# Performance work log

Measured on AMD Instinct MI355X. Metric: run time of the kernel, lower is better.

## Reference

```python
import jax, jax.numpy as jnp
import numpy as np

B, C, H, W = 16, 192, 48, 48
EPS = 1e-5  # torch LayerNorm default


def setup_inputs() -> dict:
    key = jax.random.key(0)
    ks = jax.random.split(key, 5)
    dim = C
    x = jax.random.normal(ks[0], (B, C, H, W), dtype=jnp.float32)
    ln_w = jnp.ones((dim,), dtype=jnp.float32)
    ln_b = jnp.zeros((dim,), dtype=jnp.float32)
    s = 1.0 / np.sqrt(dim)
    Wq = jax.random.uniform(ks[1], (dim, dim), jnp.float32, -s, s)
    Wk = jax.random.uniform(ks[2], (dim, dim), jnp.float32, -s, s)
    Wv = jax.random.uniform(ks[3], (dim, dim), jnp.float32, -s, s)
    w1 = jnp.ones((1,), dtype=jnp.float32)
    w2 = jnp.ones((1,), dtype=jnp.float32)
    return {"x": x, "ln_w": ln_w, "ln_b": ln_b, "Wq": Wq, "Wk": Wk, "Wv": Wv, "w1": w1, "w2": w2}


def reference(x, ln_w, ln_b, Wq, Wk, Wv, w1, w2):
    b, c, h, w = x.shape
    # [B, C, H, W] -> [B, N, C]
    xf = x.reshape(b, c, h * w).transpose(0, 2, 1)
    # LayerNorm over channel dim
    mu = jnp.mean(xf, axis=-1, keepdims=True)
    var = jnp.mean(jnp.square(xf - mu), axis=-1, keepdims=True)
    xn = (xf - mu) * jax.lax.rsqrt(var + EPS) * ln_w + ln_b
    # torch Linear: y = x @ W^T
    Q = jnp.einsum('bnc,dc->bnd', xn, Wq)
    K = jnp.einsum('bnc,dc->bnd', xn, Wk)
    V = jnp.einsum('bnc,dc->bnd', xn, Wv)
    S = jnp.einsum('bnd,bmd->bnm', Q, K)  # [B, N, N]
    attn1 = jax.nn.softmax(S, axis=-1)
    attn2 = jnp.square(jax.nn.relu(S))
    # learned blend weights (softmax over two scalars)
    e1, e2 = jnp.exp(w1), jnp.exp(w2)
    denom = e1 + e2
    attn = (e1 / denom) * attn1 + (e2 / denom) * attn2
    out = jnp.einsum('bnm,bmd->bnd', attn, V)  # [B, N, C]
    out = out.transpose(0, 2, 1).reshape(b, c, h, w)
    return out + x
```

## Files before the change

### kernel.cpp

```cpp
#include <hip/hip_runtime.h>

#define NN 2304
#define CC 192
#define NBATCH 16

typedef unsigned short u16;
typedef __bf16 bf16x8 __attribute__((ext_vector_type(8)));
typedef float f32x4 __attribute__((ext_vector_type(4)));
typedef float f32x16 __attribute__((ext_vector_type(16)));

__device__ __forceinline__ u16 bf16bits(float f) {
  union { float f; unsigned u; } v;
  v.f = f;
  unsigned r = v.u + 0x7FFFu + ((v.u >> 16) & 1u);
  return (u16)(r >> 16);
}

__device__ __forceinline__ uint32_t cvtpk(float lo, float hi) {
  uint32_t d;
  asm("v_cvt_pk_bf16_f32 %0, %1, %2" : "=v"(d) : "v"(lo), "v"(hi));
  return d;
}

__device__ __forceinline__ int swzK(int row, int col) {
  int ch = col >> 3;
  int phys = (ch & ~7) | ((ch ^ row) & 7);
  return row * 192 + (phys << 3) + (col & 7);
}
__device__ __forceinline__ int swz64(int row, int col) {
  int ch = (col >> 3) ^ row;
  return (row << 6) | ((ch & 7) << 3) | (col & 7);
}

__device__ __forceinline__ void gll16(const u16* g, u16* l) {
  __builtin_amdgcn_global_load_lds(
      (const __attribute__((address_space(1))) u16*)g,
      (__attribute__((address_space(3))) u16*)l, 16, 0, 0);
}

__global__ __launch_bounds__(256) void ln_kernel(
    const float* __restrict__ x, const float* __restrict__ lnw,
    const float* __restrict__ lnb, u16* __restrict__ xn) {
  __shared__ float xt[192 * 65];
  __shared__ float psum[4][64], psq[4][64];
  __shared__ float mu_s[64], rs_s[64];
  __shared__ float lw_s[192], lb_s[192];
  int t = threadIdx.x;
  int b = blockIdx.y, n0 = blockIdx.x * 64;
  const float* xb = x + (size_t)b * CC * NN;
  if (t < 192) { lw_s[t] = lnw[t]; lb_s[t] = lnb[t]; }
#pragma unroll
  for (int i = 0; i < 48; ++i) {
    int idx = i * 256 + t;
    int c = idx >> 6, n = idx & 63;
    xt[c * 65 + n] = xb[(size_t)c * NN + n0 + n];
  }
  __syncthreads();
  {
    int n = t & 63, part = t >> 6;
    float s = 0.f, s2 = 0.f;
#pragma unroll
    for (int c = part * 48; c < part * 48 + 48; ++c) {
      float v = xt[c * 65 + n];
      s += v; s2 += v * v;
    }
    psum[part][n] = s; psq[part][n] = s2;
  }
  __syncthreads();
  if (t < 64) {
    float s = psum[0][t] + psum[1][t] + psum[2][t] + psum[3][t];
    float s2 = psq[0][t] + psq[1][t] + psq[2][t] + psq[3][t];
    float mu = s * (1.0f / 192.0f);
    float var = s2 * (1.0f / 192.0f) - mu * mu;
    mu_s[t] = mu;
    rs_s[t] = rsqrtf(var + 1e-5f);
  }
  __syncthreads();
#pragma unroll
  for (int i = 0; i < 12; ++i) {
    int u = i * 256 + t;
    int n = u / 48, cq = (u % 48) * 4;
    float mu = mu_s[n], rs = rs_s[n];
    float v0 = (xt[(cq + 0) * 65 + n] - mu) * rs * lw_s[cq + 0] + lb_s[cq + 0];
    float v1 = (xt[(cq + 1) * 65 + n] - mu) * rs * lw_s[cq + 1] + lb_s[cq + 1];
    float v2 = (xt[(cq + 2) * 65 + n] - mu) * rs * lw_s[cq + 2] + lb_s[cq + 2];
    float v3 = (xt[(cq + 3) * 65 + n] - mu) * rs * lw_s[cq + 3] + lb_s[cq + 3];
    uint2 o;
    o.x = cvtpk(v0, v1);
    o.y = cvtpk(v2, v3);
    *(uint2*)&xn[((size_t)(b * NN + n0 + n)) * CC + cq] = o;
  }
}

__global__ __launch_bounds__(256, 3) void qkv_gemm(
    const u16* __restrict__ xn, const float* __restrict__ Wq,
    const float* __restrict__ Wk, const float* __restrict__ Wv,
    u16* __restrict__ qb, u16* __restrict__ kb, u16* __restrict__ vtb) {
  __shared__ u16 xs[12288];
  __shared__ u16 wsm[12288];
  int t = threadIdx.x, w = t >> 6, lane = t & 63, l15 = lane & 15, qd = lane >> 4;
  int m0 = blockIdx.x * 64, n0 = blockIdx.y * 64, z = blockIdx.z;
  const float* W = (z == 0) ? Wq : (z == 1 ? Wk : Wv);
#pragma unroll
  for (int i = 0; i < 6; ++i) {
    int ch = i * 256 + t;
    int row = ch / 24, cin = (ch % 24) * 8;
    *(uint4*)&xs[swzK(row, cin)] = *(const uint4*)&xn[(size_t)(m0 + row) * 192 + cin];
  }
#pragma unroll
  for (int i = 0; i < 6; ++i) {
    int ch = i * 256 + t;
    int row = ch / 24, cin = (ch % 24) * 8;
    const float* src = &W[(size_t)(n0 + row) * 192 + cin];
    float4 f0 = *(const float4*)src;
    float4 f1 = *(const float4*)(src + 4);
    uint4 o;
    o.x = cvtpk(f0.x, f0.y);
    o.y = cvtpk(f0.z, f0.w);
    o.z = cvtpk(f1.x, f1.y);
    o.w = cvtpk(f1.z, f1.w);
    *(uint4*)&wsm[swzK(row, cin)] = o;
  }
  __syncthreads();
  bf16x8 a[6];
#pragma unroll
  for (int kk = 0; kk < 6; ++kk)
    a[kk] = *(const bf16x8*)&xs[swzK(w * 16 + l15, kk * 32 + qd * 8)];
  const f32x4 fz = {0.f, 0.f, 0.f, 0.f};
  f32x4 acc[4];
#pragma unroll
  for (int ct = 0; ct < 4; ++ct) {
    acc[ct] = fz;
#pragma unroll
    for (int kk = 0; kk < 6; ++kk) {
      bf16x8 bfr = *(const bf16x8*)&wsm[swzK(ct * 16 + l15, kk * 32 + qd * 8)];
      acc[ct] = __builtin_amdgcn_mfma_f32_16x16x32_bf16(a[kk], bfr, acc[ct], 0, 0, 0);
    }
  }
  if (z < 2) {
    u16* outp = (z == 0) ? qb : kb;
#pragma unroll
    for (int ct = 0; ct < 4; ++ct)
#pragma unroll
      for (int r = 0; r < 4; ++r) {
        int m = m0 + w * 16 + qd * 4 + r;
        outp[(size_t)m * 192 + n0 + ct * 16 + l15] = bf16bits(acc[ct][r]);
      }
  } else {
    __syncthreads();
#pragma unroll
    for (int ct = 0; ct < 4; ++ct)
#pragma unroll
      for (int r = 0; r < 4; ++r)
        xs[swz64(ct * 16 + l15, w * 16 + qd * 4 + r)] = bf16bits(acc[ct][r]);
    __syncthreads();
    int b = blockIdx.x / 36, nb = (blockIdx.x % 36) * 64;
#pragma unroll
    for (int i = 0; i < 16; ++i) {
      int idx = i * 256 + t;
      int d = idx >> 6, nn = idx & 63;
      vtb[(size_t)b * 192 * NN + (size_t)(n0 + d) * NN + nb + nn] = xs[swz64(d, nn)];
    }
  }
}

__global__ __launch_bounds__(256, 2) void attn_fused(
    const u16* __restrict__ qb, const u16* __restrict__ kb,
    const u16* __restrict__ vtb, const float* __restrict__ w1p,
    const float* __restrict__ w2p, const float* __restrict__ x,
    float* __restrict__ out) {
  __shared__ u16 sm[32768];
  float* olds = (float*)sm;
  float* lred = (float*)(sm + 24576);

  int t = threadIdx.x, w = t >> 6, lane = t & 63;
  int l31 = lane & 31, hi = lane >> 5;
  int qh = w >> 1, ch = w & 1;
  int bid = blockIdx.x;
  int xcd = bid & 7, j = bid >> 3;
  int b = xcd * 2 + (j >= 36 ? 1 : 0);
  int qt = (j >= 36) ? j - 36 : j;

  const u16* Kg = kb + (size_t)b * NN * CC;
  const u16* Vg = vtb + (size_t)b * CC * NN;
  const u16* Qr = qb + ((size_t)b * NN + qt * 64 + qh * 32 + l31) * CC + hi * 8;
  bf16x8 qf[12];
#pragma unroll
  for (int ks = 0; ks < 12; ++ks) qf[ks] = *(const bf16x8*)(Qr + ks * 16);

  float e1 = __expf(w1p[0]), e2 = __expf(w2p[0]);
  float den = e1 + e2;
  float c1f = e1 / den, c2f = e2 / den;

  u16* pexSW = sm + 24576 + (qh * 2 + ch) * 1024 + lane * 8;
  const u16* pexSR = sm + 24576 + (qh * 2 + (1 - ch)) * 1024 + lane * 8;
  u16* pexRW = sm + 28672 + (qh * 2 + ch) * 1024 + lane * 8;
  const u16* pexRR = sm + 28672 + (qh * 2 + (1 - ch)) * 1024 + lane * 8;

  f32x16 z16;
#pragma unroll
  for (int i = 0; i < 16; ++i) z16[i] = 0.f;
  f32x16 os[3], orl[3];
#pragma unroll
  for (int i = 0; i < 3; ++i) { os[i] = z16; orl[i] = z16; }
  float lsum = 0.f;

#define STAGE_K(KT)                                                        \
  {                                                                        \
    _Pragma("unroll") for (int i = 0; i < 6; ++i) {                        \
      int cid = i * 4 + w, sc = cid * 64 + lane;                           \
      int row = sc / 24, pc = sc % 24;                                     \
      int gc = (pc & ~7) | ((pc ^ row) & 7);                               \
      gll16(Kg + ((size_t)(KT) * 64 + row) * CC + gc * 8, sm + cid * 512); \
    }                                                                      \
  }
#define STAGE_V(KT)                                                        \
  {                                                                        \
    _Pragma("unroll") for (int i = 0; i < 6; ++i) {                        \
      int cid = i * 4 + w, sc = cid * 64 + lane;                           \
      int d = sc >> 3, pc = sc & 7, gc = (pc ^ d) & 7;                     \
      gll16(Vg + (size_t)d * NN + (KT) * 64 + gc * 8,                      \
            sm + 12288 + cid * 512);                                       \
    }                                                                      \
  }

  alignas(16) uint32_t pS0[4], pS1[4], pR0[4], pR1[4];
#define S_BLEND()                                                           \
  {                                                                         \
    f32x16 sA0 = z16, sA1 = z16;                                            \
    __builtin_amdgcn_s_setprio(1);                                          \
    _Pragma("unroll") for (int ks = 0; ks < 6; ++ks) {                      \
      bf16x8 k0 =                                                           \
          *(const bf16x8*)&sm[swzK(ch * 32 + l31, (2 * ks) * 16 + hi * 8)]; \
      bf16x8 k1 =                                                           \
          *(const bf16x8*)&sm[swzK(ch * 32 + l31, (2 * ks + 1) * 16 + hi * 8)]; \
      sA0 = __builtin_amdgcn_mfma_f32_32x32x16_bf16(k0, qf[2 * ks], sA0, 0, 0, 0); \
      sA1 = __builtin_amdgcn_mfma_f32_32x32x16_bf16(k1, qf[2 * ks + 1], sA1, 0, 0, 0); \
    }                                                                       \
    __builtin_amdgcn_s_setprio(0);                                          \
    uint32_t WS[8], WR[8];                                                  \
    _Pragma("unroll") for (int g = 0; g < 4; ++g) {                         \
      float sv0 = sA0[4 * g + 0] + sA1[4 * g + 0];                          \
      float sv1 = sA0[4 * g + 1] + sA1[4 * g + 1];                          \
      float sv2 = sA0[4 * g + 2] + sA1[4 * g + 2];                          \
      float sv3 = sA0[4 * g + 3] + sA1[4 * g + 3];                          \
      float e0 = __expf(fminf(sv0, 60.f));                                  \
      float e1v = __expf(fminf(sv1, 60.f));                                 \
      float e2v = __expf(fminf(sv2, 60.f));                                 \
      float e3 = __expf(fminf(sv3, 60.f));                                  \
      float r0 = fmaxf(sv0, 0.f), r1 = fmaxf(sv1, 0.f);                     \
      float r2 = fmaxf(sv2, 0.f), r3 = fmaxf(sv3, 0.f);                     \
      lsum += (e0 + e1v) + (e2v + e3);                                      \
      WS[2 * g] = cvtpk(e0, e1v);                                           \
      WS[2 * g + 1] = cvtpk(e2v, e3);                                       \
      WR[2 * g] = cvtpk(r0 * r0, r1 * r1);                                  \
      WR[2 * g + 1] = cvtpk(r2 * r2, r3 * r3);                              \
    }                                                                       \
    uint32_t XS[8], XR[8];                                                  \
    _Pragma("unroll") for (int jj = 0; jj < 8; ++jj) {                      \
      XS[jj] = __shfl_xor(WS[jj], 32);                                      \
      XR[jj] = __shfl_xor(WR[jj], 32);                                      \
    }                                                                       \
    pS0[0] = hi ? XS[2] : WS[0]; pS0[1] = hi ? XS[3] : WS[1];               \
    pS0[2] = hi ? WS[2] : XS[0]; pS0[3] = hi ? WS[3] : XS[1];               \
    pS1[0] = hi ? XS[6] : WS[4]; pS1[1] = hi ? XS[7] : WS[5];               \
    pS1[2] = hi ? WS[6] : XS[4]; pS1[3] = hi ? WS[7] : XS[5];               \
    pR0[0] = hi ? XR[2] : WR[0]; pR0[1] = hi ? XR[3] : WR[1];               \
    pR0[2] = hi ? WR[2] : XR[0]; pR0[3] = hi ? WR[3] : XR[1];               \
    pR1[0] = hi ? XR[6] : WR[4]; pR1[1] = hi ? XR[7] : WR[5];               \
    pR1[2] = hi ? WR[6] : XR[4]; pR1[3] = hi ? WR[7] : XR[5];               \
    *(uint4*)pexSW = *(uint4*)pS0;                                          \
    *(uint4*)(pexSW + 512) = *(uint4*)pS1;                                  \
    *(uint4*)pexRW = *(uint4*)pR0;                                          \
    *(uint4*)(pexRW + 512) = *(uint4*)pR1;                                  \
  }

  STAGE_K(0);
  STAGE_V(0);
  asm volatile("s_waitcnt vmcnt(6)\ns_barrier" ::: "memory");
  S_BLEND();
  asm volatile("s_waitcnt lgkmcnt(0)\ns_barrier" ::: "memory");
  STAGE_K(1);

  for (int kt = 0; kt < 36; ++kt) {
    if (kt == 35)
      asm volatile("s_waitcnt vmcnt(0) lgkmcnt(0)\ns_barrier" ::: "memory");
    else
      asm volatile("s_waitcnt vmcnt(6) lgkmcnt(0)\ns_barrier" ::: "memory");

    const u16* vl = sm + 12288;
    uint4 sS0 = *(const uint4*)pexSR;
    uint4 sS1 = *(const uint4*)(pexSR + 512);
    uint4 sR0 = *(const uint4*)pexRR;
    uint4 sR1 = *(const uint4*)(pexRR + 512);
    __builtin_amdgcn_s_setprio(1);
#pragma unroll
    for (int dt = 0; dt < 3; ++dt) {
      int d = ch * 96 + dt * 32 + l31;
      bf16x8 vo0 = *(const bf16x8*)&vl[swz64(d, (ch * 2 + 0) * 16 + hi * 8)];
      bf16x8 vo1 = *(const bf16x8*)&vl[swz64(d, (ch * 2 + 1) * 16 + hi * 8)];
      bf16x8 vs0 = *(const bf16x8*)&vl[swz64(d, ((1 - ch) * 2 + 0) * 16 + hi * 8)];
      bf16x8 vs1 = *(const bf16x8*)&vl[swz64(d, ((1 - ch) * 2 + 1) * 16 + hi * 8)];
      os[dt] = __builtin_amdgcn_mfma_f32_32x32x16_bf16(
          *(const bf16x8*)pS0, vo0, os[dt], 0, 0, 0);
      orl[dt] = __builtin_amdgcn_mfma_f32_32x32x16_bf16(
          *(const bf16x8*)pR0, vo0, orl[dt], 0, 0, 0);
      os[dt] = __builtin_amdgcn_mfma_f32_32x32x16_bf16(
          *(const bf16x8*)pS1, vo1, os[dt], 0, 0, 0);
      orl[dt] = __builtin_amdgcn_mfma_f32_32x32x16_bf16(
          *(const bf16x8*)pR1, vo1, orl[dt], 0, 0, 0);
      os[dt] = __builtin_amdgcn_mfma_f32_32x32x16_bf16(
          *(const bf16x8*)&sS0, vs0, os[dt], 0, 0, 0);
      orl[dt] = __builtin_amdgcn_mfma_f32_32x32x16_bf16(
          *(const bf16x8*)&sR0, vs0, orl[dt], 0, 0, 0);
      os[dt] = __builtin_amdgcn_mfma_f32_32x32x16_bf16(
          *(const bf16x8*)&sS1, vs1, os[dt], 0, 0, 0);
      orl[dt] = __builtin_amdgcn_mfma_f32_32x32x16_bf16(
          *(const bf16x8*)&sR1, vs1, orl[dt], 0, 0, 0);
    }
    __builtin_amdgcn_s_setprio(0);

    if (kt < 35) {
      asm volatile("s_waitcnt vmcnt(0) lgkmcnt(0)\ns_barrier" ::: "memory");
      STAGE_V(kt + 1);
      S_BLEND();
      asm volatile("s_waitcnt lgkmcnt(0)\ns_barrier" ::: "memory");
      if (kt + 2 < 36) STAGE_K(kt + 2);
    }
  }

  lsum += __shfl_xor(lsum, 32);
  __syncthreads();
  if (lane < 32) lred[(qh * 2 + ch) * 32 + l31] = lsum;
  __syncthreads();
  float linv[16];
#pragma unroll
  for (int r = 0; r < 16; ++r) {
    int m = (r & 3) + 8 * (r >> 2) + 4 * hi;
    float ltot = lred[(qh * 2 + 0) * 32 + m] + lred[(qh * 2 + 1) * 32 + m];
    linv[r] = c1f / ltot;
  }
  __syncthreads();
#pragma unroll
  for (int dt = 0; dt < 3; ++dt) {
    int d = ch * 96 + dt * 32 + l31;
#pragma unroll
    for (int r = 0; r < 16; ++r) {
      int m = (r & 3) + 8 * (r >> 2) + 4 * hi;
      int q = qh * 32 + m;
      olds[d * 64 + ((q & ~31) | ((q ^ d) & 31))] =
          os[dt][r] * linv[r] + c2f * orl[dt][r];
    }
  }
  __syncthreads();
  const float* xb = x + (size_t)b * CC * NN + qt * 64;
  float* ob = out + (size_t)b * CC * NN + qt * 64;
#pragma unroll
  for (int i = 0; i < 48; ++i) {
    int idx = i * 256 + t;
    int c = idx >> 6, nn = idx & 63;
    float v = olds[c * 64 + ((nn & ~31) | ((nn ^ c) & 31))];
    ob[(size_t)c * NN + nn] = v + xb[(size_t)c * NN + nn];
  }
#undef STAGE_K
#undef STAGE_V
#undef S_BLEND
}

extern "C" void kernel_launch(void* const* d_in, const int* in_sizes, int n_in,
                              void* d_out, int out_size, void* d_ws, size_t ws_size,
                              hipStream_t stream) {
  (void)in_sizes; (void)n_in; (void)out_size; (void)ws_size;
  const float* x   = (const float*)d_in[0];
  const float* lnw = (const float*)d_in[1];
  const float* lnb = (const float*)d_in[2];
  const float* Wq  = (const float*)d_in[3];
  const float* Wk  = (const float*)d_in[4];
  const float* Wv  = (const float*)d_in[5];
  const float* w1  = (const float*)d_in[6];
  const float* w2  = (const float*)d_in[7];
  float* out = (float*)d_out;

  u16* xn = (u16*)d_ws;
  size_t per = (size_t)NBATCH * NN * CC;
  u16* qb  = xn + per;
  u16* kb  = qb + per;
  u16* vtb = kb + per;

  ln_kernel<<<dim3(36, 16), 256, 0, stream>>>(x, lnw, lnb, xn);
  qkv_gemm<<<dim3(576, 3, 3), 256, 0, stream>>>(xn, Wq, Wk, Wv, qb, kb, vtb);
  attn_fused<<<dim3(576), 256, 0, stream>>>(qb, kb, vtb, w1, w2, x, out);
}
```

Baseline: 283.1 us.

## Pre-convert QKV weights to bf16 and loop Q/K/V inside one GEMM block

Adds a small kernel that converts Wq/Wk/Wv to bf16 once. The QKV GEMM then processes all three projections in one block, reusing the staged xn tile and A fragments. Tiles are loaded with direct global-to-LDS loads (gll16) using a swizzle, and the next weight tile is prefetched while the current outputs are written. This removes the repeated fp32 weight conversion and triples xn reuse, at the cost of an extra launch and fewer, longer blocks.

Result: no change. 285.9 us (+1.0%).

```diff
diff --git a/kernel.cpp b/kernel.cpp
--- a/kernel.cpp
+++ b/kernel.cpp
@@ -92,74 +92,97 @@
   }
 }
 
+__global__ __launch_bounds__(256) void wconv_kernel(
+    const float* __restrict__ Wq, const float* __restrict__ Wk,
+    const float* __restrict__ Wv, u16* __restrict__ wbf) {
+  int z = blockIdx.y;
+  const float* W = (z == 0) ? Wq : (z == 1 ? Wk : Wv);
+  u16* o = wbf + (size_t)z * 36864;
+  int idx = (blockIdx.x * 256 + (int)threadIdx.x) * 8;
+  float4 f0 = *(const float4*)&W[idx];
+  float4 f1 = *(const float4*)&W[idx + 4];
+  uint4 v;
+  v.x = cvtpk(f0.x, f0.y);
+  v.y = cvtpk(f0.z, f0.w);
+  v.z = cvtpk(f1.x, f1.y);
+  v.w = cvtpk(f1.z, f1.w);
+  *(uint4*)&o[idx] = v;
+}
+
 __global__ __launch_bounds__(256, 3) void qkv_gemm(
-    const u16* __restrict__ xn, const float* __restrict__ Wq,
-    const float* __restrict__ Wk, const float* __restrict__ Wv,
+    const u16* __restrict__ xn, const u16* __restrict__ wbf,
     u16* __restrict__ qb, u16* __restrict__ kb, u16* __restrict__ vtb) {
   __shared__ u16 xs[12288];
   __shared__ u16 wsm[12288];
   int t = threadIdx.x, w = t >> 6, lane = t & 63, l15 = lane & 15, qd = lane >> 4;
-  int m0 = blockIdx.x * 64, n0 = blockIdx.y * 64, z = blockIdx.z;
-  const float* W = (z == 0) ? Wq : (z == 1 ? Wk : Wv);
+  int m0 = blockIdx.x * 64, n0 = blockIdx.y * 64;
+
 #pragma unroll
   for (int i = 0; i < 6; ++i) {
-    int ch = i * 256 + t;
-    int row = ch / 24, cin = (ch % 24) * 8;
-    *(uint4*)&xs[swzK(row, cin)] = *(const uint4*)&xn[(size_t)(m0 + row) * 192 + cin];
+    int cid = i * 4 + w, sc = cid * 64 + lane;
+    int row = sc / 24, pc = sc % 24;
+    int gc = (pc & ~7) | ((pc ^ row) & 7);
+    gll16(xn + (size_t)(m0 + row) * 192 + gc * 8, xs + cid * 512);
   }
 #pragma unroll
   for (int i = 0; i < 6; ++i) {
-    int ch = i * 256 + t;
-    int row = ch / 24, cin = (ch % 24) * 8;
-    const float* src = &W[(size_t)(n0 + row) * 192 + cin];
-    float4 f0 = *(const float4*)src;
-    float4 f1 = *(const float4*)(src + 4);
-    uint4 o;
-    o.x = cvtpk(f0.x, f0.y);
-    o.y = cvtpk(f0.z, f0.w);
-    o.z = cvtpk(f1.x, f1.y);
-    o.w = cvtpk(f1.z, f1.w);
-    *(uint4*)&wsm[swzK(row, cin)] = o;
-  }
-  __syncthreads();
+    int cid = i * 4 + w, sc = cid * 64 + lane;
+    int row = sc / 24, pc = sc % 24;
+    int gc = (pc & ~7) | ((pc ^ row) & 7);
+    gll16(wbf + (size_t)(n0 + row) * 192 + gc * 8, wsm + cid * 512);
+  }
+
   bf16x8 a[6];
-#pragma unroll
-  for (int kk = 0; kk < 6; ++kk)
-    a[kk] = *(const bf16x8*)&xs[swzK(w * 16 + l15, kk * 32 + qd * 8)];
   const f32x4 fz = {0.f, 0.f, 0.f, 0.f};
-  f32x4 acc[4];
-#pragma unroll
-  for (int ct = 0; ct < 4; ++ct) {
-    acc[ct] = fz;
-#pragma unroll
-    for (int kk = 0; kk < 6; ++kk) {
-      bf16x8 bfr = *(const bf16x8*)&wsm[swzK(ct * 16 + l15, kk * 32 + qd * 8)];
-      acc[ct] = __builtin_amdgcn_mfma_f32_16x16x32_bf16(a[kk], bfr, acc[ct], 0, 0, 0);
-    }
-  }
-  if (z < 2) {
-    u16* outp = (z == 0) ? qb : kb;
-#pragma unroll
-    for (int ct = 0; ct < 4; ++ct)
-#pragma unroll
-      for (int r = 0; r < 4; ++r) {
-        int m = m0 + w * 16 + qd * 4 + r;
-        outp[(size_t)m * 192 + n0 + ct * 16 + l15] = bf16bits(acc[ct][r]);
+  for (int z = 0; z < 3; ++z) {
+    asm volatile("s_waitcnt vmcnt(0) lgkmcnt(0)\ns_barrier" ::: "memory");
+    if (z == 0) {
+#pragma unroll
+      for (int kk = 0; kk < 6; ++kk)
+        a[kk] = *(const bf16x8*)&xs[swzK(w * 16 + l15, kk * 32 + qd * 8)];
+    }
+    f32x4 acc[4];
+#pragma unroll
+    for (int ct = 0; ct < 4; ++ct) {
+      acc[ct] = fz;
+#pragma unroll
+      for (int kk = 0; kk < 6; ++kk) {
+        bf16x8 bfr = *(const bf16x8*)&wsm[swzK(ct * 16 + l15, kk * 32 + qd * 8)];
+        acc[ct] = __builtin_amdgcn_mfma_f32_16x16x32_bf16(a[kk], bfr, acc[ct], 0, 0, 0);
       }
-  } else {
-    __syncthreads();
-#pragma unroll
-    for (int ct = 0; ct < 4; ++ct)
-#pragma unroll
-      for (int r = 0; r < 4; ++r)
-        xs[swz64(ct * 16 + l15, w * 16 + qd * 4 + r)] = bf16bits(acc[ct][r]);
-    __syncthreads();
-    int b = blockIdx.x / 36, nb = (blockIdx.x % 36) * 64;
-#pragma unroll
-    for (int i = 0; i < 16; ++i) {
-      int idx = i * 256 + t;
-      int d = idx >> 6, nn = idx & 63;
-      vtb[(size_t)b * 192 * NN + (size_t)(n0 + d) * NN + nb + nn] = xs[swz64(d, nn)];
+    }
+    asm volatile("s_waitcnt lgkmcnt(0)\ns_barrier" ::: "memory");
+    if (z < 2) {
+#pragma unroll
+      for (int i = 0; i < 6; ++i) {
+        int cid = i * 4 + w, sc = cid * 64 + lane;
+        int row = sc / 24, pc = sc % 24;
+        int gc = (pc & ~7) | ((pc ^ row) & 7);
+        gll16(wbf + (size_t)(z + 1) * 36864 + (size_t)(n0 + row) * 192 + gc * 8,
+              wsm + cid * 512);
+      }
+      u16* outp = (z == 0) ? qb : kb;
+#pragma unroll
+      for (int ct = 0; ct < 4; ++ct)
+#pragma unroll
+        for (int r = 0; r < 4; ++r) {
+          int m = m0 + w * 16 + qd * 4 + r;
+          outp[(size_t)m * 192 + n0 + ct * 16 + l15] = bf16bits(acc[ct][r]);
+        }
+    } else {
+#pragma unroll
+      for (int ct = 0; ct < 4; ++ct)
+#pragma unroll
+        for (int r = 0; r < 4; ++r)
+          xs[swz64(ct * 16 + l15, w * 16 + qd * 4 + r)] = bf16bits(acc[ct][r]);
+      __syncthreads();
+      int bb = blockIdx.x / 36, nb = (blockIdx.x % 36) * 64;
+#pragma unroll
+      for (int i = 0; i < 16; ++i) {
+        int idx = i * 256 + t;
+        int d = idx >> 6, nn = idx & 63;
+        vtb[(size_t)bb * 192 * NN + (size_t)(n0 + d) * NN + nb + nn] = xs[swz64(d, nn)];
+      }
     }
   }
 }
@@ -386,8 +409,10 @@
   u16* qb  = xn + per;
   u16* kb  = qb + per;
   u16* vtb = kb + per;
+  u16* wbf = vtb + per;
 
   ln_kernel<<<dim3(36, 16), 256, 0, stream>>>(x, lnw, lnb, xn);
-  qkv_gemm<<<dim3(576, 3, 3), 256, 0, stream>>>(xn, Wq, Wk, Wv, qb, kb, vtb);
+  wconv_kernel<<<dim3(18, 3), 256, 0, stream>>>(Wq, Wk, Wv, wbf);
+  qkv_gemm<<<dim3(576, 3), 256, 0, stream>>>(xn, wbf, qb, kb, vtb);
   attn_fused<<<dim3(576), 256, 0, stream>>>(qb, kb, vtb, w1, w2, x, out);
 }
```
